# Kernel tuning notes

Hardware: AMD Instinct MI355X
Metric: run time of the kernel (lower is better)

The kernel has to match this reference:

```python
import jax, jax.numpy as jnp
import numpy as np

VOCAB_BLOCK = 2048
TEMP = 1.0
EPS_LO = 0.2
EPS_HI = 0.3


def setup_inputs() -> dict:
    key = jax.random.key(0)
    k = jax.random.split(key, 6)
    B, S, D, V = 4, 1024, 2048, 32768
    hidden_states = jax.random.normal(k[0], (B, S, D), dtype=jnp.float32)
    # 0.02 init scale keeps logits O(1) so exp/logsumexp stay well-conditioned
    lm_head_kernel = jax.random.normal(k[1], (D, V), dtype=jnp.float32) * 0.02
    input_ids = jax.random.randint(k[2], (B, S), 0, V, dtype=jnp.int32)
    labels = jax.random.randint(k[3], (B, S), 0, 2, dtype=jnp.int32)
    advantages = jax.random.normal(k[4], (B,), dtype=jnp.float32)
    old_per_token_logps = jax.random.normal(k[5], (B, S - 1), dtype=jnp.float32) * 0.1
    return {
        "hidden_states": hidden_states,
        "lm_head_kernel": lm_head_kernel,
        "input_ids": input_ids,
        "labels": labels,
        "advantages": advantages,
        "old_per_token_logps": old_per_token_logps,
    }


def _fused_logps(h, kernel):
    """Streaming logsumexp over vocab blocks; never materializes [B,T,V]."""
    B, T, D = h.shape
    V = kernel.shape[1]
    nb = V // VOCAB_BLOCK
    Wb = kernel.reshape(D, nb, VOCAB_BLOCK).transpose(1, 0, 2)  # [nb, D, bs]

    def step(carry, wb):
        m, s = carry
        lg = jnp.einsum("btd,dv->btv", h, wb) / TEMP  # [B,T,bs]
        bm = lg.max(axis=-1)
        nm = jnp.maximum(m, bm)
        s = s * jnp.exp(m - nm) + jnp.exp(lg - nm[..., None]).sum(axis=-1)
        return (nm, s), None

    init = (jnp.full((B, T), -jnp.inf, dtype=h.dtype), jnp.zeros((B, T), dtype=h.dtype))
    (m, s), _ = jax.lax.scan(step, init, Wb)
    return m + jnp.log(s)  # logsumexp over full vocab, [B,T]


def reference(hidden_states, lm_head_kernel, input_ids, labels, advantages, old_per_token_logps):
    h = hidden_states[:, :-1, :]            # [B,T,D], T = S-1
    chosen = input_ids[:, 1:]               # [B,T]
    mask = labels[:, 1:].astype(jnp.float32)

    # chosen-token logit: gather kernel columns, no full logits tensor
    w_sel = lm_head_kernel.T[chosen]        # [B,T,D]
    chosen_logit = jnp.einsum("btd,btd->bt", h, w_sel) / TEMP

    lse = _fused_logps(h, lm_head_kernel)
    per_token_logps = chosen_logit - lse    # [B,T]

    ratio = jnp.exp(per_token_logps - old_per_token_logps)
    adv = advantages[:, None]
    loss1 = ratio * adv
    loss2 = jnp.clip(ratio, 1.0 - EPS_LO, 1.0 + EPS_HI) * adv
    per_token_loss = -jnp.minimum(loss1, loss2)

    total_valid = mask.sum()
    loss = (per_token_loss * mask).sum() / total_valid
    return loss, jax.lax.stop_gradient(per_token_logps)
```

## Files before the change

kernel.cpp:

```cpp
#include <hip/hip_runtime.h>
#include <hip/hip_bf16.h>

typedef unsigned short u16;
typedef unsigned char u8;
typedef unsigned long long u64;
typedef __attribute__((ext_vector_type(4))) int i32x4;
typedef __attribute__((ext_vector_type(8))) int i32x8;
typedef __attribute__((ext_vector_type(4))) float f32x4;

#define NROWS 4092
#define NROWS_PAD 4096
#define DDIM 2048
#define VDIM 32768
#define NCHUNK 512
#define SC8 0x7F7F7F7F

__device__ __forceinline__ u8 f2fp8(float f) {
  union { float f; unsigned u; } v; v.f = f;
  unsigned s = (v.u >> 24) & 0x80u;
  unsigned a = v.u & 0x7FFFFFFFu;
  if (a >= 0x43E80000u) return (u8)(s | 0x7E);
  int e = (int)(a >> 23) - 127;
  unsigned m = a & 0x7FFFFFu;
  if (e < -6) {
    unsigned full = m | 0x800000u;
    int sh = 20 + (-6 - e);
    if (sh > 31) return (u8)s;
    unsigned q = full >> sh;
    unsigned rem = full & ((1u << sh) - 1u), half = 1u << (sh - 1);
    q += (rem > half || (rem == half && (q & 1u)));
    return (u8)(s | q);
  }
  unsigned q = m >> 20, rem = m & 0xFFFFFu;
  q += (rem > 0x80000u || (rem == 0x80000u && (q & 1u)));
  unsigned bits = (((unsigned)(e + 7)) << 3) + q;
  if (bits >= 0x7Fu) bits = 0x7Eu;
  return (u8)(s | bits);
}

__device__ __forceinline__ void gload16(const void* g, void* l) {
  using gp_t = const __attribute__((address_space(1))) unsigned*;
  using lp_t = __attribute__((address_space(3))) unsigned*;
  __builtin_amdgcn_global_load_lds((gp_t)g, (lp_t)(unsigned)(unsigned long long)l,
                                   16, 0, 0);
}

#define BAR() __builtin_amdgcn_s_barrier()
#define SB()  __builtin_amdgcn_sched_barrier(0)
#define SHUF(a, b) __builtin_shufflevector(a, b, 0, 1, 2, 3, 4, 5, 6, 7)

__global__ void init_k(const int* __restrict__ ids, int* __restrict__ chosen,
                       float* __restrict__ chlog, float* __restrict__ accum) {
  int i = blockIdx.x * 256 + threadIdx.x;
  if (i < NROWS_PAD) {
    int v = -1;
    if (i < NROWS) { int b = i / 1023, t = i % 1023; v = ids[b * 1024 + t + 1]; }
    chosen[i] = v;
    chlog[i] = 0.f;
  }
  if (i < 2) accum[i] = 0.f;
}

__global__ void bucket_k(const int* __restrict__ chosen,
                         int* __restrict__ boff, int* __restrict__ bent) {
  __shared__ int cnt[512];
  __shared__ int base[512];
  int tid = threadIdx.x;
  cnt[tid] = 0;
  __syncthreads();
  int loc[8], tile[8];
#pragma unroll
  for (int j = 0; j < 8; ++j) {
    int r = tid + (j << 9);
    int c = chosen[r];
    int ti = (c < 0) ? 512 : (c >> 6);
    tile[j] = ti;
    loc[j] = (ti < 512) ? atomicAdd(&cnt[ti], 1) : 0;
  }
  __syncthreads();
  if (tid == 0) {
    int s = 0;
    for (int i = 0; i < 512; ++i) { base[i] = s; s += cnt[i]; }
  }
  __syncthreads();
  boff[tid] = base[tid];
  if (tid == 511) boff[512] = base[511] + cnt[511];
#pragma unroll
  for (int j = 0; j < 8; ++j) {
    int r = tid + (j << 9);
    if (tile[j] < 512) bent[base[tile[j]] + loc[j]] = (r << 6) | (chosen[r] & 63);
  }
}

__global__ void conv_h(const float* __restrict__ hs, u8* __restrict__ h8) {
  int idx = blockIdx.x * 256 + threadIdx.x;
  int row = idx >> 8;
  int c8 = (idx & 255) << 3;
  u64 o = 0;
  if (row < NROWS) {
    int b = row / 1023, t = row % 1023;
    const float* p = hs + (size_t)((b << 10) + t) * DDIM + c8;
    float4 x = *(const float4*)p, y = *(const float4*)(p + 4);
    o = (u64)f2fp8(x.x * 16.f)        | ((u64)f2fp8(x.y * 16.f) << 8) |
        ((u64)f2fp8(x.z * 16.f) << 16) | ((u64)f2fp8(x.w * 16.f) << 24) |
        ((u64)f2fp8(y.x * 16.f) << 32) | ((u64)f2fp8(y.y * 16.f) << 40) |
        ((u64)f2fp8(y.z * 16.f) << 48) | ((u64)f2fp8(y.w * 16.f) << 56);
  }
  *(u64*)(h8 + (size_t)row * DDIM + c8) = o;
}

__global__ void transpose_w(const float* __restrict__ W, u8* __restrict__ WT8,
                            const float* __restrict__ hs,
                            const int* __restrict__ boff,
                            const int* __restrict__ bent,
                            float* __restrict__ chlog) {
  __shared__ float t32[64][65];
  __shared__ u8 t8[64][68];
  int v0 = blockIdx.x << 6, d0 = blockIdx.y << 6;
  int tid = threadIdx.x;
  int vi = (tid & 15) << 2, dl = tid >> 4;
#pragma unroll
  for (int i = 0; i < 4; ++i) {
    int d = dl + (i << 4);
    float4 w = *(const float4*)(W + (size_t)(d0 + d) * VDIM + v0 + vi);
    t32[d][vi + 0] = w.x; t32[d][vi + 1] = w.y;
    t32[d][vi + 2] = w.z; t32[d][vi + 3] = w.w;
    t8[d][vi + 0] = f2fp8(w.x * 64.f); t8[d][vi + 1] = f2fp8(w.y * 64.f);
    t8[d][vi + 2] = f2fp8(w.z * 64.f); t8[d][vi + 3] = f2fp8(w.w * 64.f);
  }
  __syncthreads();
  int vr = tid >> 2, dc = (tid & 3) << 4;
  union { u8 b[16]; ulonglong2 q; } u;
#pragma unroll
  for (int k = 0; k < 16; ++k) u.b[k] = t8[dc + k][vr];
  *(ulonglong2*)(WT8 + (size_t)(v0 + vr) * DDIM + d0 + dc) = u.q;
  int m0 = boff[blockIdx.x], m1 = boff[blockIdx.x + 1];
  int lane = tid & 63, wv = tid >> 6;
  for (int m = m0 + wv; m < m1; m += 4) {
    int e = bent[m];
    int r = e >> 6, cv = e & 63;
    int b = r / 1023, tt = r % 1023;
    float s = hs[(size_t)((b << 10) + tt) * DDIM + d0 + lane] * t32[lane][cv];
#pragma unroll
    for (int o = 1; o < 64; o <<= 1) s += __shfl_xor(s, o, 64);
    if (lane == 0) atomicAdd(chlog + r, s);
  }
}

__global__ __launch_bounds__(512, 2) void gemm_lse(
    const u8* __restrict__ A, const u8* __restrict__ Bt,
    float2* __restrict__ partials) {
  extern __shared__ u16 smem[];
  char* lds = (char*)smem;

  const int tid = threadIdx.x;
  const int l = tid & 63;
  const int wid = tid >> 6;
  const int wm = wid >> 2, wn = wid & 3;
  const int ln = l & 15;
  const int g4 = l >> 4;
  const int xr = ln & 7;

  int bid = blockIdx.x;
  int id = ((bid & 7) << 8) | (bid >> 3);
  int bm = id & 15;
  int bn = id >> 4;
  const int m0 = bm << 8, n0 = bn << 8;

  const u8* Ab = A + (size_t)m0 * DDIM;
  const u8* Bb = Bt + (size_t)n0 * DDIM;

  const unsigned aA0 = (wm << 14) + (ln << 7) + ((((g4 << 1) | 0) ^ xr) << 4);
  const unsigned aA1 = (wm << 14) + (ln << 7) + ((((g4 << 1) | 1) ^ xr) << 4);
  const unsigned aB0 = 32768u + ((wn >> 1) << 14) + ((((wn & 1) << 6) | ln) << 7) + ((((g4 << 1) | 0) ^ xr) << 4);
  const unsigned aB1 = 32768u + ((wn >> 1) << 14) + ((((wn & 1) << 6) | ln) << 7) + ((((g4 << 1) | 1) ^ xr) << 4);

  const int srow = l >> 3;
  const unsigned selb = (unsigned)(((l & 7) ^ srow) << 4);
  const unsigned voff0 = (unsigned)(((wid << 3) | srow) * 2048) + selb;
  const unsigned voff1 = (unsigned)((((8 + wid) << 3) | srow) * 2048) + selb;
  const int w10 = wid << 10;

#define RFL(x) __builtin_amdgcn_readfirstlane((int)(x))
#define GLL(src, dst) gload16((src), lds + RFL(dst))
#define LD4(off) (*(const i32x4*)(lds + (off)))
#define FRAG(b0, b1, o) SHUF(LD4((b0) + (o)), LD4((b1) + (o)))

#define MFMA_PH(q, A0, A1) do {                                                \
    __builtin_amdgcn_s_setprio(1);                                             \
    _Pragma("unroll")                                                          \
    for (int _ni = 0; _ni < 4; ++_ni)                                          \
      acc[(q) * 2][_ni] = __builtin_amdgcn_mfma_scale_f32_16x16x128_f8f6f4(    \
          (A0), bf[_ni], acc[(q) * 2][_ni], 0, 0, 0, SC8, 0, SC8);             \
    _Pragma("unroll")                                                          \
    for (int _ni = 0; _ni < 4; ++_ni)                                          \
      acc[(q) * 2 + 1][_ni] = __builtin_amdgcn_mfma_scale_f32_16x16x128_f8f6f4(\
          (A1), bf[_ni], acc[(q) * 2 + 1][_ni], 0, 0, 0, SC8, 0, SC8);         \
    __builtin_amdgcn_s_setprio(0);                                             \
  } while (0)

  f32x4 acc[8][4] = {};

  GLL(Ab + voff0, w10);                    GLL(Ab + voff1, w10 + 8192);
  GLL(Ab + 262144 + voff0, w10 + 16384);   GLL(Ab + 262144 + voff1, w10 + 24576);
  GLL(Bb + voff0, w10 + 32768);            GLL(Bb + voff1, w10 + 40960);
  GLL(Bb + 262144 + voff0, w10 + 49152);   GLL(Bb + 262144 + voff1, w10 + 57344);
  GLL(Bb + 128 + voff0, w10 + 98304);      GLL(Bb + 128 + voff1, w10 + 106496);
  GLL(Bb + 128 + 262144 + voff0, w10 + 114688);
  GLL(Bb + 128 + 262144 + voff1, w10 + 122880);
  asm volatile("s_waitcnt vmcnt(4)" ::: "memory"); SB();
  BAR();
  SB();

  for (int t = 0; t < 16; ++t) {
    const unsigned fb = (unsigned)((t & 1) << 16);
    const unsigned fbn = fb ^ 65536u;
    const u8* baseA = Ab + ((t + 1) << 7);
    const u8* baseB = Bb + ((t + 2) << 7);
    const unsigned rA0 = fb + aA0, rA1 = fb + aA1;
    const unsigned rB0 = fb + aB0, rB1 = fb + aB1;

    i32x8 bf[4];
#pragma unroll
    for (int ni = 0; ni < 4; ++ni) bf[ni] = FRAG(rB0, rB1, ni * 2048);

    i32x8 a0 = FRAG(rA0, rA1, 0), a1 = FRAG(rA0, rA1, 2048);
    if (t < 15) { GLL(baseA + voff0, fbn + w10); GLL(baseA + voff1, fbn + w10 + 8192); }
    MFMA_PH(0, a0, a1);
    a0 = FRAG(rA0, rA1, 4096); a1 = FRAG(rA0, rA1, 6144);
    if (t < 15) { GLL(baseA + 262144 + voff0, fbn + w10 + 16384);
                  GLL(baseA + 262144 + voff1, fbn + w10 + 24576); }
    MFMA_PH(1, a0, a1);
    SB();
    BAR();
    a0 = FRAG(rA0, rA1, 8192); a1 = FRAG(rA0, rA1, 10240);
    if (t < 14) { GLL(baseB + voff0, fb + w10 + 32768);
                  GLL(baseB + voff1, fb + w10 + 40960); }
    MFMA_PH(2, a0, a1);
    a0 = FRAG(rA0, rA1, 12288); a1 = FRAG(rA0, rA1, 14336);
    if (t < 14) { GLL(baseB + 262144 + voff0, fb + w10 + 49152);
                  GLL(baseB + 262144 + voff1, fb + w10 + 57344); }
    MFMA_PH(3, a0, a1);
    if (t < 14)       { asm volatile("s_waitcnt vmcnt(4)" ::: "memory"); }
    else if (t == 14) { asm volatile("s_waitcnt vmcnt(0)" ::: "memory"); }
    SB();
    BAR();
    SB();
  }

  const int chunk = (bn << 2) | wn;
#pragma unroll
  for (int mi = 0; mi < 8; ++mi) {
#pragma unroll
    for (int rr = 0; rr < 4; ++rr) {
      const int row = m0 + (wm << 7) + (mi << 4) + (g4 << 2) + rr;
      float v0 = acc[mi][0][rr] * 0.0009765625f;
      float v1 = acc[mi][1][rr] * 0.0009765625f;
      float v2 = acc[mi][2][rr] * 0.0009765625f;
      float v3 = acc[mi][3][rr] * 0.0009765625f;
      float mx = fmaxf(fmaxf(v0, v1), fmaxf(v2, v3));
#pragma unroll
      for (int o = 1; o < 16; o <<= 1) mx = fmaxf(mx, __shfl_xor(mx, o, 64));
      float s = __expf(v0 - mx) + __expf(v1 - mx) + __expf(v2 - mx) + __expf(v3 - mx);
#pragma unroll
      for (int o = 1; o < 16; o <<= 1) s += __shfl_xor(s, o, 64);
      if (ln == 0) partials[(size_t)row * NCHUNK + chunk] = make_float2(mx, s);
    }
  }
#undef MFMA_PH
#undef FRAG
#undef LD4
#undef GLL
#undef RFL
}

__global__ void reduce_lse(const float2* __restrict__ partials,
                           const float* __restrict__ chlog,
                           const float* __restrict__ oldlp,
                           const int* __restrict__ labels,
                           const float* __restrict__ adv,
                           float* __restrict__ out, float* __restrict__ accum) {
  const int wid = threadIdx.x >> 6, l = threadIdx.x & 63;
  const int row = blockIdx.x * 4 + wid;
  float M = -INFINITY, S = 0.f;
  for (int c = l; c < NCHUNK; c += 64) {
    float2 p = partials[(size_t)row * NCHUNK + c];
    float Mn = fmaxf(M, p.x);
    S = S * __expf(M - Mn) + p.y * __expf(p.x - Mn);
    M = Mn;
  }
#pragma unroll
  for (int o = 1; o < 64; o <<= 1) {
    float Mo = __shfl_xor(M, o, 64), So = __shfl_xor(S, o, 64);
    float Mn = fmaxf(M, Mo);
    S = S * __expf(M - Mn) + So * __expf(Mo - Mn);
    M = Mn;
  }
  if (l == 0) {
    float lse = M + __logf(S);
    float ptl = chlog[row] - lse;
    out[1 + row] = ptl;
    int b = row / 1023, t = row % 1023;
    float a = adv[b];
    float ratio = __expf(ptl - oldlp[row]);
    float l1 = ratio * a;
    float l2 = fminf(fmaxf(ratio, 0.8f), 1.3f) * a;
    float mk = (float)labels[b * 1024 + t + 1];
    atomicAdd(accum + 0, -fminf(l1, l2) * mk);
    atomicAdd(accum + 1, mk);
  }
}

__global__ void finalize_k(const float* __restrict__ accum, float* __restrict__ out) {
  out[0] = accum[0] / accum[1];
}

extern "C" void kernel_launch(void* const* d_in, const int* in_sizes, int n_in,
                              void* d_out, int out_size, void* d_ws, size_t ws_size,
                              hipStream_t stream) {
  const float* hs     = (const float*)d_in[0];
  const float* W      = (const float*)d_in[1];
  const int*   ids    = (const int*)d_in[2];
  const int*   labels = (const int*)d_in[3];
  const float* adv    = (const float*)d_in[4];
  const float* oldlp  = (const float*)d_in[5];
  float* out = (float*)d_out;

  char* ws = (char*)d_ws;
  u8*     WT8      = (u8*)ws;
  u8*     h8       = (u8*)(ws + 67108864);
  float2* partials = (float2*)(ws + 75497472);
  float*  chlog    = (float*)(ws + 92274688);
  int*    chosen   = (int*)(ws + 92291072);
  float*  accum    = (float*)(ws + 92307456);
  int*    boff     = (int*)(ws + 92307520);
  int*    bent     = (int*)(ws + 92309632);

  (void)hipFuncSetAttribute((const void*)gemm_lse,
                            hipFuncAttributeMaxDynamicSharedMemorySize, 131072);

  init_k<<<16, 256, 0, stream>>>(ids, chosen, chlog, accum);
  bucket_k<<<1, 512, 0, stream>>>(chosen, boff, bent);
  conv_h<<<4096, 256, 0, stream>>>(hs, h8);
  transpose_w<<<dim3(512, 32), 256, 0, stream>>>(W, WT8, hs, boff, bent, chlog);
  gemm_lse<<<2048, 512, 131072, stream>>>(h8, WT8, partials);
  reduce_lse<<<1023, 256, 0, stream>>>(partials, chlog, oldlp, labels, adv, out, accum);
  finalize_k<<<1, 1, 0, stream>>>(accum, out);
}
```

Measured before the change: 574.7 us.

## Shrink GEMM tile to 128x256 with smaller LDS double buffer

Reworks the fp8 GEMM+LSE kernel from a 256x256 block tile to a 128x256 tile. The LDS double-buffer layout and per-wave A/B fragment offsets change to match, each wave now holds a 4x4 accumulator set instead of 8x4, and the launch grid doubles to 4096 blocks. LDS per block drops from 128KB to 96KB, which lowers register and LDS pressure and may allow more resident blocks. In exchange, arithmetic intensity per block falls and the B tile is re-read from memory twice as often.

```diff
diff --git a/kernel.cpp b/kernel.cpp
--- a/kernel.cpp
+++ b/kernel.cpp
@@ -14,6 +14,7 @@
 #define VDIM 32768
 #define NCHUNK 512
 #define SC8 0x7F7F7F7F
+#define BUFB 49152u
 
 __device__ __forceinline__ u8 f2fp8(float f) {
   union { float f; unsigned u; } v; v.f = f;
@@ -156,29 +157,31 @@
   const int tid = threadIdx.x;
   const int l = tid & 63;
   const int wid = tid >> 6;
-  const int wm = wid >> 2, wn = wid & 3;
+  const int wmr = wid >> 2, wnr = wid & 3;
   const int ln = l & 15;
   const int g4 = l >> 4;
   const int xr = ln & 7;
 
   int bid = blockIdx.x;
-  int id = ((bid & 7) << 8) | (bid >> 3);
-  int bm = id & 15;
-  int bn = id >> 4;
-  const int m0 = bm << 8, n0 = bn << 8;
+  int id = ((bid & 7) << 9) | (bid >> 3);
+  int bm = id & 31;
+  int bn = id >> 5;
+  const int m0 = bm << 7, n0 = bn << 8;
 
   const u8* Ab = A + (size_t)m0 * DDIM;
   const u8* Bb = Bt + (size_t)n0 * DDIM;
 
-  const unsigned aA0 = (wm << 14) + (ln << 7) + ((((g4 << 1) | 0) ^ xr) << 4);
-  const unsigned aA1 = (wm << 14) + (ln << 7) + ((((g4 << 1) | 1) ^ xr) << 4);
-  const unsigned aB0 = 32768u + ((wn >> 1) << 14) + ((((wn & 1) << 6) | ln) << 7) + ((((g4 << 1) | 0) ^ xr) << 4);
-  const unsigned aB1 = 32768u + ((wn >> 1) << 14) + ((((wn & 1) << 6) | ln) << 7) + ((((g4 << 1) | 1) ^ xr) << 4);
+  const unsigned aA0 = (unsigned)(((wmr << 6) | ln) << 7) + ((((g4 << 1) | 0) ^ xr) << 4);
+  const unsigned aA1 = (unsigned)(((wmr << 6) | ln) << 7) + ((((g4 << 1) | 1) ^ xr) << 4);
+  const unsigned aB0 = 16384u + (unsigned)(((wnr << 6) | ln) << 7) + ((((g4 << 1) | 0) ^ xr) << 4);
+  const unsigned aB1 = 16384u + (unsigned)(((wnr << 6) | ln) << 7) + ((((g4 << 1) | 1) ^ xr) << 4);
 
   const int srow = l >> 3;
   const unsigned selb = (unsigned)(((l & 7) ^ srow) << 4);
-  const unsigned voff0 = (unsigned)(((wid << 3) | srow) * 2048) + selb;
-  const unsigned voff1 = (unsigned)((((8 + wid) << 3) | srow) * 2048) + selb;
+  const unsigned voff0 = (unsigned)((((0  + wid) << 3) | srow) * 2048) + selb;
+  const unsigned voff1 = (unsigned)((((8  + wid) << 3) | srow) * 2048) + selb;
+  const unsigned voff2 = (unsigned)((((16 + wid) << 3) | srow) * 2048) + selb;
+  const unsigned voff3 = (unsigned)((((24 + wid) << 3) | srow) * 2048) + selb;
   const int w10 = wid << 10;
 
 #define RFL(x) __builtin_amdgcn_readfirstlane((int)(x))
@@ -186,35 +189,31 @@
 #define LD4(off) (*(const i32x4*)(lds + (off)))
 #define FRAG(b0, b1, o) SHUF(LD4((b0) + (o)), LD4((b1) + (o)))
 
-#define MFMA_PH(q, A0, A1) do {                                                \
+#define MFMA4(q, af) do {                                                      \
     __builtin_amdgcn_s_setprio(1);                                             \
     _Pragma("unroll")                                                          \
     for (int _ni = 0; _ni < 4; ++_ni)                                          \
-      acc[(q) * 2][_ni] = __builtin_amdgcn_mfma_scale_f32_16x16x128_f8f6f4(    \
-          (A0), bf[_ni], acc[(q) * 2][_ni], 0, 0, 0, SC8, 0, SC8);             \
-    _Pragma("unroll")                                                          \
-    for (int _ni = 0; _ni < 4; ++_ni)                                          \
-      acc[(q) * 2 + 1][_ni] = __builtin_amdgcn_mfma_scale_f32_16x16x128_f8f6f4(\
-          (A1), bf[_ni], acc[(q) * 2 + 1][_ni], 0, 0, 0, SC8, 0, SC8);         \
+      acc[(q)][_ni] = __builtin_amdgcn_mfma_scale_f32_16x16x128_f8f6f4(        \
+          (af), bf[_ni], acc[(q)][_ni], 0, 0, 0, SC8, 0, SC8);                 \
     __builtin_amdgcn_s_setprio(0);                                             \
   } while (0)
 
-  f32x4 acc[8][4] = {};
-
-  GLL(Ab + voff0, w10);                    GLL(Ab + voff1, w10 + 8192);
-  GLL(Ab + 262144 + voff0, w10 + 16384);   GLL(Ab + 262144 + voff1, w10 + 24576);
-  GLL(Bb + voff0, w10 + 32768);            GLL(Bb + voff1, w10 + 40960);
-  GLL(Bb + 262144 + voff0, w10 + 49152);   GLL(Bb + 262144 + voff1, w10 + 57344);
-  GLL(Bb + 128 + voff0, w10 + 98304);      GLL(Bb + 128 + voff1, w10 + 106496);
-  GLL(Bb + 128 + 262144 + voff0, w10 + 114688);
-  GLL(Bb + 128 + 262144 + voff1, w10 + 122880);
+  f32x4 acc[4][4] = {};
+
+  GLL(Ab + voff0, w10);                 GLL(Ab + voff1, 8192 + w10);
+  GLL(Bb + voff0, 16384 + w10);         GLL(Bb + voff1, 24576 + w10);
+  GLL(Bb + voff2, 32768 + w10);         GLL(Bb + voff3, 40960 + w10);
+  GLL(Bb + 128 + voff0, BUFB + 16384 + w10);
+  GLL(Bb + 128 + voff1, BUFB + 24576 + w10);
+  GLL(Bb + 128 + voff2, BUFB + 32768 + w10);
+  GLL(Bb + 128 + voff3, BUFB + 40960 + w10);
   asm volatile("s_waitcnt vmcnt(4)" ::: "memory"); SB();
   BAR();
   SB();
 
   for (int t = 0; t < 16; ++t) {
-    const unsigned fb = (unsigned)((t & 1) << 16);
-    const unsigned fbn = fb ^ 65536u;
+    const unsigned fb = (unsigned)(t & 1) * BUFB;
+    const unsigned fbn = BUFB - fb;
     const u8* baseA = Ab + ((t + 1) << 7);
     const u8* baseB = Bb + ((t + 2) << 7);
     const unsigned rA0 = fb + aA0, rA1 = fb + aA1;
@@ -224,23 +223,23 @@
 #pragma unroll
     for (int ni = 0; ni < 4; ++ni) bf[ni] = FRAG(rB0, rB1, ni * 2048);
 
-    i32x8 a0 = FRAG(rA0, rA1, 0), a1 = FRAG(rA0, rA1, 2048);
-    if (t < 15) { GLL(baseA + voff0, fbn + w10); GLL(baseA + voff1, fbn + w10 + 8192); }
-    MFMA_PH(0, a0, a1);
-    a0 = FRAG(rA0, rA1, 4096); a1 = FRAG(rA0, rA1, 6144);
-    if (t < 15) { GLL(baseA + 262144 + voff0, fbn + w10 + 16384);
-                  GLL(baseA + 262144 + voff1, fbn + w10 + 24576); }
-    MFMA_PH(1, a0, a1);
+    i32x8 af = FRAG(rA0, rA1, 0);
+    if (t < 15) GLL(baseA + voff0, fbn + w10);
+    MFMA4(0, af);
+    af = FRAG(rA0, rA1, 2048);
+    if (t < 15) GLL(baseA + voff1, fbn + 8192 + w10);
+    MFMA4(1, af);
     SB();
     BAR();
-    a0 = FRAG(rA0, rA1, 8192); a1 = FRAG(rA0, rA1, 10240);
-    if (t < 14) { GLL(baseB + voff0, fb + w10 + 32768);
-                  GLL(baseB + voff1, fb + w10 + 40960); }
-    MFMA_PH(2, a0, a1);
-    a0 = FRAG(rA0, rA1, 12288); a1 = FRAG(rA0, rA1, 14336);
-    if (t < 14) { GLL(baseB + 262144 + voff0, fb + w10 + 49152);
-                  GLL(baseB + 262144 + voff1, fb + w10 + 57344); }
-    MFMA_PH(3, a0, a1);
+    SB();
+    af = FRAG(rA0, rA1, 4096);
+    if (t < 14) { GLL(baseB + voff0, fb + 16384 + w10);
+                  GLL(baseB + voff1, fb + 24576 + w10); }
+    MFMA4(2, af);
+    af = FRAG(rA0, rA1, 6144);
+    if (t < 14) { GLL(baseB + voff2, fb + 32768 + w10);
+                  GLL(baseB + voff3, fb + 40960 + w10); }
+    MFMA4(3, af);
     if (t < 14)       { asm volatile("s_waitcnt vmcnt(4)" ::: "memory"); }
     else if (t == 14) { asm volatile("s_waitcnt vmcnt(0)" ::: "memory"); }
     SB();
@@ -248,12 +247,12 @@
     SB();
   }
 
-  const int chunk = (bn << 2) | wn;
-#pragma unroll
-  for (int mi = 0; mi < 8; ++mi) {
+  const int chunk = (bn << 2) | wnr;
+#pragma unroll
+  for (int mi = 0; mi < 4; ++mi) {
 #pragma unroll
     for (int rr = 0; rr < 4; ++rr) {
-      const int row = m0 + (wm << 7) + (mi << 4) + (g4 << 2) + rr;
+      const int row = m0 + (wmr << 6) + (mi << 4) + (g4 << 2) + rr;
       float v0 = acc[mi][0][rr] * 0.0009765625f;
       float v1 = acc[mi][1][rr] * 0.0009765625f;
       float v2 = acc[mi][2][rr] * 0.0009765625f;
@@ -267,7 +266,7 @@
       if (ln == 0) partials[(size_t)row * NCHUNK + chunk] = make_float2(mx, s);
     }
   }
-#undef MFMA_PH
+#undef MFMA4
 #undef FRAG
 #undef LD4
 #undef GLL
@@ -337,13 +336,13 @@
   int*    bent     = (int*)(ws + 92309632);
 
   (void)hipFuncSetAttribute((const void*)gemm_lse,
-                            hipFuncAttributeMaxDynamicSharedMemorySize, 131072);
+                            hipFuncAttributeMaxDynamicSharedMemorySize, 98304);
 
   init_k<<<16, 256, 0, stream>>>(ids, chosen, chlog, accum);
   bucket_k<<<1, 512, 0, stream>>>(chosen, boff, bent);
   conv_h<<<4096, 256, 0, stream>>>(hs, h8);
   transpose_w<<<dim3(512, 32), 256, 0, stream>>>(W, WT8, hs, boff, bent, chlog);
-  gemm_lse<<<2048, 512, 131072, stream>>>(h8, WT8, partials);
+  gemm_lse<<<4096, 512, 98304, stream>>>(h8, WT8, partials);
   reduce_lse<<<1023, 256, 0, stream>>>(partials, chlog, oldlp, labels, adv, out, accum);
   finalize_k<<<1, 1, 0, stream>>>(accum, out);
 }
```

After: 564.7 us. About the same (-1.7%).

## Use 4 waves with 128x128 warp tiles in the FP8 GEMM-LSE kernel

Applied to the files above, without the earlier changes.

Restructures the fused FP8 GEMM plus partial-logsumexp kernel from 8 waves per 256x256 block (128x64 per wave) to 4 waves (128x128 per wave, 8x8 MFMA accumulators). Each A fragment now feeds 8 MFMAs, which cuts LDS fragment reads per MFMA. The prefetch is simplified to a plain double buffer for A and B with one full vmcnt wait per K step. The cost is twice as many accumulator registers per wave, lower occupancy (launch bounds 256,1), and less latency hiding, since the staggered B prefetch is gone.

```diff
diff --git a/kernel.cpp b/kernel.cpp
--- a/kernel.cpp
+++ b/kernel.cpp
@@ -14,6 +14,7 @@
 #define VDIM 32768
 #define NCHUNK 512
 #define SC8 0x7F7F7F7F
+#define BUFB 65536u
 
 __device__ __forceinline__ u8 f2fp8(float f) {
   union { float f; unsigned u; } v; v.f = f;
@@ -147,7 +148,7 @@
   }
 }
 
-__global__ __launch_bounds__(512, 2) void gemm_lse(
+__global__ __launch_bounds__(256, 1) void gemm_lse(
     const u8* __restrict__ A, const u8* __restrict__ Bt,
     float2* __restrict__ partials) {
   extern __shared__ u16 smem[];
@@ -156,7 +157,7 @@
   const int tid = threadIdx.x;
   const int l = tid & 63;
   const int wid = tid >> 6;
-  const int wm = wid >> 2, wn = wid & 3;
+  const int wmr = wid >> 1, wnr = wid & 1;
   const int ln = l & 15;
   const int g4 = l >> 4;
   const int xr = ln & 7;
@@ -170,104 +171,94 @@
   const u8* Ab = A + (size_t)m0 * DDIM;
   const u8* Bb = Bt + (size_t)n0 * DDIM;
 
-  const unsigned aA0 = (wm << 14) + (ln << 7) + ((((g4 << 1) | 0) ^ xr) << 4);
-  const unsigned aA1 = (wm << 14) + (ln << 7) + ((((g4 << 1) | 1) ^ xr) << 4);
-  const unsigned aB0 = 32768u + ((wn >> 1) << 14) + ((((wn & 1) << 6) | ln) << 7) + ((((g4 << 1) | 0) ^ xr) << 4);
-  const unsigned aB1 = 32768u + ((wn >> 1) << 14) + ((((wn & 1) << 6) | ln) << 7) + ((((g4 << 1) | 1) ^ xr) << 4);
+  const unsigned aA0 = (unsigned)((wmr << 14) + (ln << 7)) + (((0 | g4) ^ xr) << 4);
+  const unsigned aA1 = (unsigned)((wmr << 14) + (ln << 7)) + (((4 | g4) ^ xr) << 4);
+  const unsigned aB0 = 32768u + (unsigned)((wnr << 14) + (ln << 7)) + (((0 | g4) ^ xr) << 4);
+  const unsigned aB1 = 32768u + (unsigned)((wnr << 14) + (ln << 7)) + (((4 | g4) ^ xr) << 4);
 
   const int srow = l >> 3;
   const unsigned selb = (unsigned)(((l & 7) ^ srow) << 4);
-  const unsigned voff0 = (unsigned)(((wid << 3) | srow) * 2048) + selb;
-  const unsigned voff1 = (unsigned)((((8 + wid) << 3) | srow) * 2048) + selb;
-  const int w10 = wid << 10;
+  unsigned voff[8];
+#pragma unroll
+  for (int j = 0; j < 8; ++j)
+    voff[j] = (unsigned)(((((j << 2) + wid) << 3) | srow) * 2048) + selb;
 
 #define RFL(x) __builtin_amdgcn_readfirstlane((int)(x))
 #define GLL(src, dst) gload16((src), lds + RFL(dst))
 #define LD4(off) (*(const i32x4*)(lds + (off)))
 #define FRAG(b0, b1, o) SHUF(LD4((b0) + (o)), LD4((b1) + (o)))
-
-#define MFMA_PH(q, A0, A1) do {                                                \
-    __builtin_amdgcn_s_setprio(1);                                             \
-    _Pragma("unroll")                                                          \
-    for (int _ni = 0; _ni < 4; ++_ni)                                          \
-      acc[(q) * 2][_ni] = __builtin_amdgcn_mfma_scale_f32_16x16x128_f8f6f4(    \
-          (A0), bf[_ni], acc[(q) * 2][_ni], 0, 0, 0, SC8, 0, SC8);             \
-    _Pragma("unroll")                                                          \
-    for (int _ni = 0; _ni < 4; ++_ni)                                          \
-      acc[(q) * 2 + 1][_ni] = __builtin_amdgcn_mfma_scale_f32_16x16x128_f8f6f4(\
-          (A1), bf[_ni], acc[(q) * 2 + 1][_ni], 0, 0, 0, SC8, 0, SC8);         \
-    __builtin_amdgcn_s_setprio(0);                                             \
-  } while (0)
-
-  f32x4 acc[8][4] = {};
-
-  GLL(Ab + voff0, w10);                    GLL(Ab + voff1, w10 + 8192);
-  GLL(Ab + 262144 + voff0, w10 + 16384);   GLL(Ab + 262144 + voff1, w10 + 24576);
-  GLL(Bb + voff0, w10 + 32768);            GLL(Bb + voff1, w10 + 40960);
-  GLL(Bb + 262144 + voff0, w10 + 49152);   GLL(Bb + 262144 + voff1, w10 + 57344);
-  GLL(Bb + 128 + voff0, w10 + 98304);      GLL(Bb + 128 + voff1, w10 + 106496);
-  GLL(Bb + 128 + 262144 + voff0, w10 + 114688);
-  GLL(Bb + 128 + 262144 + voff1, w10 + 122880);
-  asm volatile("s_waitcnt vmcnt(4)" ::: "memory"); SB();
+#define DSTA(j) (unsigned)((((j) << 2) + wid) << 10)
+#define DSTB(j) (32768u + (unsigned)((((j) << 2) + wid) << 10))
+
+  f32x4 acc[8][8] = {};
+
+#pragma unroll
+  for (int j = 0; j < 8; ++j) GLL(Ab + voff[j], DSTA(j));
+#pragma unroll
+  for (int j = 0; j < 8; ++j) GLL(Bb + voff[j], DSTB(j));
+  asm volatile("s_waitcnt vmcnt(0)" ::: "memory"); SB();
   BAR();
   SB();
 
   for (int t = 0; t < 16; ++t) {
-    const unsigned fb = (unsigned)((t & 1) << 16);
-    const unsigned fbn = fb ^ 65536u;
+    const unsigned fb = (unsigned)(t & 1) * BUFB;
+    const unsigned fbn = BUFB - fb;
     const u8* baseA = Ab + ((t + 1) << 7);
-    const u8* baseB = Bb + ((t + 2) << 7);
+    const u8* baseB = Bb + ((t + 1) << 7);
     const unsigned rA0 = fb + aA0, rA1 = fb + aA1;
     const unsigned rB0 = fb + aB0, rB1 = fb + aB1;
 
-    i32x8 bf[4];
-#pragma unroll
-    for (int ni = 0; ni < 4; ++ni) bf[ni] = FRAG(rB0, rB1, ni * 2048);
-
-    i32x8 a0 = FRAG(rA0, rA1, 0), a1 = FRAG(rA0, rA1, 2048);
-    if (t < 15) { GLL(baseA + voff0, fbn + w10); GLL(baseA + voff1, fbn + w10 + 8192); }
-    MFMA_PH(0, a0, a1);
-    a0 = FRAG(rA0, rA1, 4096); a1 = FRAG(rA0, rA1, 6144);
-    if (t < 15) { GLL(baseA + 262144 + voff0, fbn + w10 + 16384);
-                  GLL(baseA + 262144 + voff1, fbn + w10 + 24576); }
-    MFMA_PH(1, a0, a1);
-    SB();
-    BAR();
-    a0 = FRAG(rA0, rA1, 8192); a1 = FRAG(rA0, rA1, 10240);
-    if (t < 14) { GLL(baseB + voff0, fb + w10 + 32768);
-                  GLL(baseB + voff1, fb + w10 + 40960); }
-    MFMA_PH(2, a0, a1);
-    a0 = FRAG(rA0, rA1, 12288); a1 = FRAG(rA0, rA1, 14336);
-    if (t < 14) { GLL(baseB + 262144 + voff0, fb + w10 + 49152);
-                  GLL(baseB + 262144 + voff1, fb + w10 + 57344); }
-    MFMA_PH(3, a0, a1);
-    if (t < 14)       { asm volatile("s_waitcnt vmcnt(4)" ::: "memory"); }
-    else if (t == 14) { asm volatile("s_waitcnt vmcnt(0)" ::: "memory"); }
+    i32x8 bf[8];
+#pragma unroll
+    for (int ni = 0; ni < 8; ++ni) bf[ni] = FRAG(rB0, rB1, ni * 2048);
+
+#pragma unroll
+    for (int mi = 0; mi < 8; ++mi) {
+      i32x8 af = FRAG(rA0, rA1, mi * 2048);
+      if (t < 15) {
+        if (mi < 4) { GLL(baseA + voff[2 * mi], fbn + DSTA(2 * mi));
+                      GLL(baseA + voff[2 * mi + 1], fbn + DSTA(2 * mi + 1)); }
+        else { int j = 2 * (mi - 4);
+               GLL(baseB + voff[j], fbn + DSTB(j));
+               GLL(baseB + voff[j + 1], fbn + DSTB(j + 1)); }
+      }
+      __builtin_amdgcn_s_setprio(1);
+#pragma unroll
+      for (int ni = 0; ni < 8; ++ni)
+        acc[mi][ni] = __builtin_amdgcn_mfma_scale_f32_16x16x128_f8f6f4(
+            af, bf[ni], acc[mi][ni], 0, 0, 0, SC8, 0, SC8);
+      __builtin_amdgcn_s_setprio(0);
+    }
+    if (t < 15) { asm volatile("s_waitcnt vmcnt(0)" ::: "memory"); }
     SB();
     BAR();
     SB();
   }
 
-  const int chunk = (bn << 2) | wn;
+  const int chunk0 = (bn << 2) | (wnr << 1);
 #pragma unroll
   for (int mi = 0; mi < 8; ++mi) {
 #pragma unroll
     for (int rr = 0; rr < 4; ++rr) {
-      const int row = m0 + (wm << 7) + (mi << 4) + (g4 << 2) + rr;
-      float v0 = acc[mi][0][rr] * 0.0009765625f;
-      float v1 = acc[mi][1][rr] * 0.0009765625f;
-      float v2 = acc[mi][2][rr] * 0.0009765625f;
-      float v3 = acc[mi][3][rr] * 0.0009765625f;
-      float mx = fmaxf(fmaxf(v0, v1), fmaxf(v2, v3));
-#pragma unroll
-      for (int o = 1; o < 16; o <<= 1) mx = fmaxf(mx, __shfl_xor(mx, o, 64));
-      float s = __expf(v0 - mx) + __expf(v1 - mx) + __expf(v2 - mx) + __expf(v3 - mx);
-#pragma unroll
-      for (int o = 1; o < 16; o <<= 1) s += __shfl_xor(s, o, 64);
-      if (ln == 0) partials[(size_t)row * NCHUNK + chunk] = make_float2(mx, s);
+      const int row = m0 + (wmr << 7) + (mi << 4) + (g4 << 2) + rr;
+#pragma unroll
+      for (int h = 0; h < 2; ++h) {
+        float v0 = acc[mi][4 * h + 0][rr] * 0.0009765625f;
+        float v1 = acc[mi][4 * h + 1][rr] * 0.0009765625f;
+        float v2 = acc[mi][4 * h + 2][rr] * 0.0009765625f;
+        float v3 = acc[mi][4 * h + 3][rr] * 0.0009765625f;
+        float mx = fmaxf(fmaxf(v0, v1), fmaxf(v2, v3));
+#pragma unroll
+        for (int o = 1; o < 16; o <<= 1) mx = fmaxf(mx, __shfl_xor(mx, o, 64));
+        float s = __expf(v0 - mx) + __expf(v1 - mx) + __expf(v2 - mx) + __expf(v3 - mx);
+#pragma unroll
+        for (int o = 1; o < 16; o <<= 1) s += __shfl_xor(s, o, 64);
+        if (ln == 0) partials[(size_t)row * NCHUNK + chunk0 + h] = make_float2(mx, s);
+      }
     }
   }
-#undef MFMA_PH
+#undef DSTA
+#undef DSTB
 #undef FRAG
 #undef LD4
 #undef GLL
@@ -343,7 +334,7 @@
   bucket_k<<<1, 512, 0, stream>>>(chosen, boff, bent);
   conv_h<<<4096, 256, 0, stream>>>(hs, h8);
   transpose_w<<<dim3(512, 32), 256, 0, stream>>>(W, WT8, hs, boff, bent, chlog);
-  gemm_lse<<<2048, 512, 131072, stream>>>(h8, WT8, partials);
+  gemm_lse<<<2048, 256, 131072, stream>>>(h8, WT8, partials);
   reduce_lse<<<1023, 256, 0, stream>>>(partials, chlog, oldlp, labels, adv, out, accum);
   finalize_k<<<1, 1, 0, stream>>>(accum, out);
 }
```

New measurement: 600.5 us. 4.5% more time.
